# Kernel optimization log

Measured on AMD Instinct MI355X. Metric: run time of the kernel, lower is better.

Reference implementation:

```python
import jax, jax.numpy as jnp
import numpy as np

N_NODES = 100000
IN_F = 128
H_F = 128
LOOKBACK = 3
N_EDGES = 640000


def setup_inputs() -> dict:
    key = jax.random.key(0)
    ks = jax.random.split(key, 16)
    s = lambda k, shp: jax.random.normal(k, shp, dtype=jnp.float32) * 0.05
    inp = {
        "feat": jax.random.normal(ks[0], (N_NODES, IN_F), dtype=jnp.float32),
        "edges": jax.random.randint(ks[1], (LOOKBACK, 2, N_EDGES), 0, N_NODES, dtype=jnp.int32),
        # conv1 (SAGEConv pool, in->h) params
        "Wp1": s(ks[2], (IN_F, IN_F)), "bp1": jnp.zeros((IN_F,), jnp.float32),
        "Ws1": s(ks[3], (H_F, IN_F)), "Wn1": s(ks[4], (H_F, IN_F)), "b1": jnp.zeros((H_F,), jnp.float32),
        # BatchNorm1d affine params (training-mode batch stats)
        "gamma": jnp.ones((H_F,), jnp.float32), "beta": jnp.zeros((H_F,), jnp.float32),
        # conv2 (SAGEConv pool, h->h) params
        "Wp2": s(ks[5], (H_F, H_F)), "bp2": jnp.zeros((H_F,), jnp.float32),
        "Ws2": s(ks[6], (H_F, H_F)), "Wn2": s(ks[7], (H_F, H_F)), "b2": jnp.zeros((H_F,), jnp.float32),
    }
    return inp


def _sage_pool_conv(h, src, dst, Wp, bp, Ws, Wn, b):
    # pool aggregator: m = relu(fc_pool(h)); neigh = max over in-edges
    m = jax.nn.relu(h @ Wp.T + bp)                      # [N, d]
    agg = jax.ops.segment_max(m[src], dst, num_segments=N_NODES)  # [N, d]
    agg = jnp.where(jnp.isfinite(agg), agg, 0.0)        # nodes with no in-edges -> 0
    return h @ Ws.T + agg @ Wn.T + b


def _batchnorm(x, gamma, beta, eps=1e-5):
    mu = jnp.mean(x, axis=0)
    var = jnp.var(x, axis=0)
    return (x - mu) * jax.lax.rsqrt(var + eps) * gamma + beta


def reference(feat, edges, Wp1, bp1, Ws1, Wn1, b1, gamma, beta, Wp2, bp2, Ws2, Wn2, b2):
    def per_graph(e):
        src, dst = e[0], e[1]
        h = _sage_pool_conv(feat, src, dst, Wp1, bp1, Ws1, Wn1, b1)
        h = _batchnorm(h, gamma, beta)
        h = jax.nn.relu(h)
        h = _sage_pool_conv(h, src, dst, Wp2, bp2, Ws2, Wn2, b2)
        return h

    return jax.vmap(per_graph)(edges)  # [lookback, N, H_F]
```

## Files before the change

kernel.cpp:

```cpp
#include <hip/hip_runtime.h>
#include <hip/hip_bf16.h>

#define NNODES 100000
#define FD 128
#define NEDGES 640000
#define NB 391
#define NT64 1563
#define GX_TWOA 170
#define GX_ONEW 340
#define GX_HEAD 512
#define OFFS_U32 100032

typedef __bf16 bf16x8 __attribute__((ext_vector_type(8)));
typedef __bf16 bf16x4 __attribute__((ext_vector_type(4)));
typedef float f32x4 __attribute__((ext_vector_type(4)));
typedef unsigned short u16x8 __attribute__((ext_vector_type(8)));

__device__ __forceinline__ bf16x8 cvt8(float4 a, float4 b) {
  bf16x8 r;
  r[0] = (__bf16)a.x; r[1] = (__bf16)a.y; r[2] = (__bf16)a.z; r[3] = (__bf16)a.w;
  r[4] = (__bf16)b.x; r[5] = (__bf16)b.y; r[6] = (__bf16)b.z; r[7] = (__bf16)b.w;
  return r;
}

__device__ __forceinline__ void gl16(const void* g, void* l) {
  __builtin_amdgcn_global_load_lds(
      (const __attribute__((address_space(1))) unsigned int*)g,
      (__attribute__((address_space(3))) unsigned int*)l, 16, 0, 0);
}

__device__ __forceinline__ void stage_abf(const __bf16* A, long row0, int M,
                                          char* l, int wid, int lane) {
#pragma unroll
  for (int i = 0; i < 2; ++i) {
    const int r0 = wid * 8 + i * 4;
    const int rl = r0 + (lane >> 4);
    long row = row0 + rl;
    if (row > M - 1) row = M - 1;
    const int slot = (lane & 15) ^ (rl & 7);
    gl16((const char*)(A + row * FD) + slot * 16, l + r0 * 256);
  }
}

__device__ __forceinline__ void stage_a32(const float* A, long row0, int M,
                                          char* l, int wid, int lane) {
#pragma unroll
  for (int i = 0; i < 4; ++i) {
    const int r0 = wid * 8 + i * 2;
    const int rl = r0 + (lane >> 5);
    long row = row0 + rl;
    if (row > M - 1) row = M - 1;
    const int slot = (lane & 31) ^ (rl & 7);
    gl16((const char*)(A + row * FD) + slot * 16, l + r0 * 512);
  }
}

__global__ __launch_bounds__(256) void packw6_k(
    const float* __restrict__ W0, const float* __restrict__ W1,
    const float* __restrict__ W2, const float* __restrict__ W3,
    const float* __restrict__ W4, const float* __restrict__ W5,
    __bf16* __restrict__ out) {
  const int gidx = blockIdx.x * 256 + threadIdx.x;
  const int wi = gidx >> 11;
  const int f = gidx & 2047;
  const float* W = wi == 0 ? W0 : wi == 1 ? W1 : wi == 2 ? W2
                 : wi == 3 ? W3 : wi == 4 ? W4 : W5;
  const int c = f >> 8, kk = (f >> 6) & 3, lane = f & 63;
  const int lr = lane & 15, lg = lane >> 4;
  const float* p = W + (c * 16 + lr) * FD + kk * 32 + lg * 8;
  *(bf16x8*)(out + (long)gidx * 8) = cvt8(*(const float4*)p, *(const float4*)(p + 4));
}

template <int AM>
__device__ __forceinline__ void lds_arow(const char* l, int rl, int lg,
                                         const float* __restrict__ scsh,
                                         bf16x8 (&af)[4]) {
#pragma unroll
  for (int kk = 0; kk < 4; ++kk) {
    if constexpr (AM == 0) {
      const int s0 = kk * 8 + lg * 2;
      const float4 x = *(const float4*)(l + rl * 512 + ((s0 + 0) ^ (rl & 7)) * 16);
      const float4 y = *(const float4*)(l + rl * 512 + ((s0 + 1) ^ (rl & 7)) * 16);
      af[kk] = cvt8(x, y);
    } else {
      const int s = kk * 4 + lg;
      const bf16x8 r = *(const bf16x8*)(l + rl * 256 + (s ^ (rl & 7)) * 16);
      if constexpr (AM == 3) {
        const int k = lg * 8 + kk * 32;
        const float4 scx = *(const float4*)(scsh + k);
        const float4 scy = *(const float4*)(scsh + k + 4);
        const float4 shx = *(const float4*)(scsh + 128 + k);
        const float4 shy = *(const float4*)(scsh + 128 + k + 4);
        bf16x8 o;
        o[0] = (__bf16)fmaxf((float)r[0] * scx.x + shx.x, 0.f);
        o[1] = (__bf16)fmaxf((float)r[1] * scx.y + shx.y, 0.f);
        o[2] = (__bf16)fmaxf((float)r[2] * scx.z + shx.z, 0.f);
        o[3] = (__bf16)fmaxf((float)r[3] * scx.w + shx.w, 0.f);
        o[4] = (__bf16)fmaxf((float)r[4] * scy.x + shy.x, 0.f);
        o[5] = (__bf16)fmaxf((float)r[5] * scy.y + shy.y, 0.f);
        o[6] = (__bf16)fmaxf((float)r[6] * scy.z + shy.z, 0.f);
        o[7] = (__bf16)fmaxf((float)r[7] * scy.w + shy.w, 0.f);
        af[kk] = o;
      } else {
        af[kk] = r;
      }
    }
  }
}

template <int A0M, int A1M, bool TWOA, bool RELU, bool OUTBF16, bool STATS,
          bool WRITEB, bool NTOUT>
__global__ __launch_bounds__(512, 2) void gemm_k(
    const void* __restrict__ A0, long a0s, const void* __restrict__ A1, long a1s,
    const __bf16* __restrict__ W0p, const __bf16* __restrict__ W1p,
    const float* __restrict__ bias, const float* __restrict__ scsh0,
    void* __restrict__ outp, long os, float* __restrict__ pblk,
    __bf16* __restrict__ bcopy, int M) {
  constexpr int ASZ = (A0M == 0) ? 32768 : 16384;
  constexpr int A1SZ = TWOA ? 16384 : 0;
  constexpr int BSZ = ASZ + A1SZ;
  constexpr int LSZ = 2 * BSZ + (STATS ? 2048 : 0);
  __shared__ __align__(16) char lds[LSZ];
  float* s_red = (float*)(lds + 2 * BSZ);

  const int g = blockIdx.y;
  const int tid = threadIdx.x;
  const int wid = tid >> 6;
  const int lane = tid & 63;
  const int rw = wid & 1;
  const int cw = wid >> 1;
  const int lr = lane & 15;
  const int lg = lane >> 4;
  const int S = gridDim.x;

  const void* A0g = (const char*)A0 + (long)g * a0s;
  const void* A1g = (const char*)A1 + (TWOA ? (long)g * a1s : 0);
  void* outg = (char*)outp + (long)g * os;
  const float* scshg = (A0M == 3 || A1M == 3) ? scsh0 + (long)g * 256 : nullptr;

  bf16x8 bw0[2][4], bw1[2][4];
#pragma unroll
  for (int ci = 0; ci < 2; ++ci)
#pragma unroll
    for (int kk = 0; kk < 4; ++kk) {
      const long f = ((long)((cw * 2 + ci) * 4 + kk) * 64 + lane) * 8;
      bw0[ci][kk] = *(const bf16x8*)(W0p + f);
      if constexpr (TWOA) bw1[ci][kk] = *(const bf16x8*)(W1p + f);
    }

  float ps[2][4], pss[2][4];
  if constexpr (STATS) {
#pragma unroll
    for (int ci = 0; ci < 2; ++ci)
#pragma unroll
      for (int j = 0; j < 4; ++j) { ps[ci][j] = 0.f; pss[ci][j] = 0.f; }
  }

  auto stageA = [&](long t, char* buf) {
    if constexpr (A0M == 0) stage_a32((const float*)A0g, t * 64, M, buf, wid, lane);
    else stage_abf((const __bf16*)A0g, t * 64, M, buf, wid, lane);
    if constexpr (TWOA) stage_abf((const __bf16*)A1g, t * 64, M, buf + ASZ, wid, lane);
  };

  auto body = [&](long t, long tn, char* cur, char* nxt) {
    if (tn < NT64) stageA(tn, nxt);

    bf16x8 a0f[2][4];
#pragma unroll
    for (int tt = 0; tt < 2; ++tt)
      lds_arow<A0M>(cur, rw * 32 + tt * 16 + lr, lg, scshg, a0f[tt]);
    bf16x8 a1f[2][4];
    if constexpr (TWOA) {
#pragma unroll
      for (int tt = 0; tt < 2; ++tt)
        lds_arow<A1M>(cur + ASZ, rw * 32 + tt * 16 + lr, lg, scshg, a1f[tt]);
    }

    if constexpr (WRITEB) {
      if (cw == 0) {
#pragma unroll
        for (int tt = 0; tt < 2; ++tt) {
          const long row = t * 64 + rw * 32 + tt * 16 + lr;
          if (row < M)
#pragma unroll
            for (int kk = 0; kk < 4; ++kk)
              *(bf16x8*)(bcopy + row * FD + lg * 8 + kk * 32) = a0f[tt][kk];
        }
      }
    }

    f32x4 acc[2][2];
#pragma unroll
    for (int tt = 0; tt < 2; ++tt)
#pragma unroll
      for (int ci = 0; ci < 2; ++ci) acc[tt][ci] = (f32x4){0.f, 0.f, 0.f, 0.f};

#pragma unroll
    for (int ci = 0; ci < 2; ++ci)
#pragma unroll
      for (int tt = 0; tt < 2; ++tt)
#pragma unroll
        for (int kk = 0; kk < 4; ++kk)
          acc[tt][ci] = __builtin_amdgcn_mfma_f32_16x16x32_bf16(bw0[ci][kk], a0f[tt][kk], acc[tt][ci], 0, 0, 0);
    if constexpr (TWOA) {
#pragma unroll
      for (int ci = 0; ci < 2; ++ci)
#pragma unroll
        for (int tt = 0; tt < 2; ++tt)
#pragma unroll
          for (int kk = 0; kk < 4; ++kk)
            acc[tt][ci] = __builtin_amdgcn_mfma_f32_16x16x32_bf16(bw1[ci][kk], a1f[tt][kk], acc[tt][ci], 0, 0, 0);
    }

#pragma unroll
    for (int tt = 0; tt < 2; ++tt) {
      const long row = t * 64 + rw * 32 + tt * 16 + lr;
      const bool ok = row < M;
      f32x4 vv[2];
#pragma unroll
      for (int ci = 0; ci < 2; ++ci) {
        const int cb = cw * 32 + ci * 16 + lg * 4;
        f32x4 v = acc[tt][ci];
        if (bias) {
          const float4 bv = *(const float4*)(bias + cb);
          v[0] += bv.x; v[1] += bv.y; v[2] += bv.z; v[3] += bv.w;
        }
        if constexpr (STATS) {
          if (ok) {
#pragma unroll
            for (int j = 0; j < 4; ++j) { ps[ci][j] += v[j]; pss[ci][j] += v[j] * v[j]; }
          }
        }
        if constexpr (RELU) {
#pragma unroll
          for (int j = 0; j < 4; ++j) v[j] = fmaxf(v[j], 0.f);
        }
        vv[ci] = v;
      }
      if constexpr (OUTBF16) {
        bf16x4 o0, o1;
#pragma unroll
        for (int j = 0; j < 4; ++j) { o0[j] = (__bf16)vv[0][j]; o1[j] = (__bf16)vv[1][j]; }
        const int2 i0 = __builtin_bit_cast(int2, o0);
        const int2 i1 = __builtin_bit_cast(int2, o1);
        int2 p0, p1;
        p0.x = __shfl_xor(i0.x, 16); p0.y = __shfl_xor(i0.y, 16);
        p1.x = __shfl_xor(i1.x, 16); p1.y = __shfl_xor(i1.y, 16);
        int4 chunk;
        int cbase;
        if ((lg & 1) == 0) {
          chunk = (int4){i0.x, i0.y, p0.x, p0.y};
          cbase = cw * 32 + lg * 4;
        } else {
          chunk = (int4){p1.x, p1.y, i1.x, i1.y};
          cbase = cw * 32 + 16 + (lg - 1) * 4;
        }
        if (ok) *(int4*)((__bf16*)outg + row * FD + cbase) = chunk;
      } else {
        if (ok) {
#pragma unroll
          for (int ci = 0; ci < 2; ++ci) {
            const int cb = cw * 32 + ci * 16 + lg * 4;
            f32x4* p = (f32x4*)((float*)outg + row * FD + cb);
            if constexpr (NTOUT) __builtin_nontemporal_store(vv[ci], p);
            else *p = vv[ci];
          }
        }
      }
    }
    __syncthreads();
  };

  long t = blockIdx.x;
  stageA(t, lds);
  __syncthreads();

  for (;;) {
    long tn = t + S;
    body(t, tn, lds, lds + BSZ);
    t = tn;
    if (t >= NT64) break;
    tn = t + S;
    body(t, tn, lds + BSZ, lds);
    t = tn;
    if (t >= NT64) break;
  }

  if constexpr (STATS) {
#pragma unroll
    for (int ci = 0; ci < 2; ++ci)
#pragma unroll
      for (int j = 0; j < 4; ++j) {
        float s = ps[ci][j], q = pss[ci][j];
        s += __shfl_xor(s, 1); s += __shfl_xor(s, 2);
        s += __shfl_xor(s, 4); s += __shfl_xor(s, 8);
        q += __shfl_xor(q, 1); q += __shfl_xor(q, 2);
        q += __shfl_xor(q, 4); q += __shfl_xor(q, 8);
        if (lr == 0) {
          s_red[(0 * 8 + wid) * 32 + ci * 16 + lg * 4 + j] = s;
          s_red[(1 * 8 + wid) * 32 + ci * 16 + lg * 4 + j] = q;
        }
      }
    __syncthreads();
    if (tid < 256) {
      const int which = tid >> 7, col = tid & 127;
      const int cwi = col >> 5, cl = col & 31;
      const float a = s_red[(which * 8 + cwi * 2 + 0) * 32 + cl] +
                      s_red[(which * 8 + cwi * 2 + 1) * 32 + cl];
      pblk[((long)g * gridDim.x + blockIdx.x) * 256 + tid] = a;
    }
  }
}

__global__ __launch_bounds__(256) void bn_final2_k(const float* __restrict__ pblk,
                                                   const float* __restrict__ gamma,
                                                   const float* __restrict__ beta,
                                                   float* __restrict__ scsh3) {
  __shared__ float s_ss[128];
  const int g = blockIdx.y;
  const int tid = threadIdx.x;
  const float* p = pblk + (long)g * GX_TWOA * 256;
  float s = 0.f;
  for (int r = 0; r < GX_TWOA; ++r) s += p[r * 256 + tid];
  if (tid >= 128) s_ss[tid - 128] = s;
  __syncthreads();
  if (tid < 128) {
    const float mu = s / (float)NNODES;
    const float var = s_ss[tid] / (float)NNODES - mu * mu;
    const float sc = rsqrtf(var + 1e-5f) * gamma[tid];
    scsh3[g * 256 + tid] = sc;
    scsh3[g * 256 + 128 + tid] = beta[tid] - mu * sc;
  }
}


__global__ __launch_bounds__(256) void hist_rank3_k(const int* __restrict__ edges,
                                                    unsigned* __restrict__ deg3,
                                                    unsigned short* __restrict__ rank3) {
  const int g = blockIdx.y;
  const int e = blockIdx.x * 256 + threadIdx.x;
  if (e < NEDGES) {
    const int d = edges[(long)g * 2 * NEDGES + NEDGES + e];
    const unsigned r = atomicAdd(&deg3[(long)g * NNODES + d], 1u);
    rank3[(long)g * NEDGES + e] = (unsigned short)r;
  }
}

__global__ __launch_bounds__(256) void blocksum3_k(const unsigned* __restrict__ deg3,
                                                   unsigned* __restrict__ bsum3) {
  __shared__ unsigned s[256];
  const int g = blockIdx.y;
  const int i = blockIdx.x * 256 + threadIdx.x;
  s[threadIdx.x] = (i < NNODES) ? deg3[(long)g * NNODES + i] : 0u;
  __syncthreads();
#pragma unroll
  for (int o = 128; o > 0; o >>= 1) {
    if (threadIdx.x < o) s[threadIdx.x] += s[threadIdx.x + o];
    __syncthreads();
  }
  if (threadIdx.x == 0) bsum3[g * NB + blockIdx.x] = s[0];
}

__global__ __launch_bounds__(512) void scanb3_k(const unsigned* __restrict__ bsum3,
                                                unsigned* __restrict__ boffs3,
                                                unsigned* __restrict__ offs3) {
  __shared__ unsigned s[512];
  const int g = blockIdx.y;
  const unsigned v = (threadIdx.x < NB) ? bsum3[g * NB + threadIdx.x] : 0u;
  s[threadIdx.x] = v;
  __syncthreads();
#pragma unroll
  for (int o = 1; o < 512; o <<= 1) {
    unsigned t = (threadIdx.x >= o) ? s[threadIdx.x - o] : 0u;
    __syncthreads();
    s[threadIdx.x] += t;
    __syncthreads();
  }
  if (threadIdx.x < NB) boffs3[g * NB + threadIdx.x] = s[threadIdx.x] - v;
  if (threadIdx.x == 0) offs3[(long)g * OFFS_U32 + NNODES] = NEDGES;
}

__global__ __launch_bounds__(256) void offsets3_k(const unsigned* __restrict__ deg3,
                                                  const unsigned* __restrict__ boffs3,
                                                  unsigned* __restrict__ offs3) {
  __shared__ unsigned s[256];
  const int g = blockIdx.y;
  const int i = blockIdx.x * 256 + threadIdx.x;
  const unsigned v = (i < NNODES) ? deg3[(long)g * NNODES + i] : 0u;
  s[threadIdx.x] = v;
  __syncthreads();
#pragma unroll
  for (int o = 1; o < 256; o <<= 1) {
    unsigned t = (threadIdx.x >= o) ? s[threadIdx.x - o] : 0u;
    __syncthreads();
    s[threadIdx.x] += t;
    __syncthreads();
  }
  const unsigned excl = s[threadIdx.x] - v + boffs3[g * NB + blockIdx.x];
  if (i < NNODES) offs3[(long)g * OFFS_U32 + i] = excl;
}

__global__ __launch_bounds__(256) void scat3_k(const int* __restrict__ edges,
                                               const unsigned* __restrict__ offs3,
                                               const unsigned short* __restrict__ rank3,
                                               int* __restrict__ ssrc3) {
  const int g = blockIdx.y;
  const int e = blockIdx.x * 256 + threadIdx.x;
  if (e < NEDGES) {
    const int s = edges[(long)g * 2 * NEDGES + e];
    const int d = edges[(long)g * 2 * NEDGES + NEDGES + e];
    const unsigned p = offs3[(long)g * OFFS_U32 + d] + rank3[(long)g * NEDGES + e];
    ssrc3[(long)g * NEDGES + p] = s;
  }
}

__global__ __launch_bounds__(256) void agg_k(const unsigned short* __restrict__ m,
                                             long ms, const int* __restrict__ ssrc3,
                                             const unsigned* __restrict__ offs3,
                                             unsigned short* __restrict__ agg3) {
  const int g = blockIdx.y;
  const unsigned short* mg = m + (long)g * ms;
  const int* ssrc = ssrc3 + (long)g * NEDGES;
  const unsigned* offs = offs3 + (long)g * OFFS_U32;
  unsigned short* agg = agg3 + (long)g * NNODES * FD;

  const int gid = blockIdx.x * 256 + threadIdx.x;
  const int node = gid >> 4;
  if (node >= NNODES) return;
  const int fl = (gid & 15) * 8;
  const unsigned beg = offs[node], end = offs[node + 1];
  u16x8 acc = {0, 0, 0, 0, 0, 0, 0, 0};
  unsigned i = beg;
  for (; i + 2 <= end; i += 2) {
    const int s0 = ssrc[i];
    const int s1 = ssrc[i + 1];
    const u16x8 v0 = *(const u16x8*)(mg + (long)s0 * FD + fl);
    const u16x8 v1 = *(const u16x8*)(mg + (long)s1 * FD + fl);
#pragma unroll
    for (int j = 0; j < 8; ++j) {
      const unsigned short mx = v0[j] > v1[j] ? v0[j] : v1[j];
      acc[j] = mx > acc[j] ? mx : acc[j];
    }
  }
  if (i < end) {
    const u16x8 v = *(const u16x8*)(mg + (long)ssrc[i] * FD + fl);
#pragma unroll
    for (int j = 0; j < 8; ++j) acc[j] = v[j] > acc[j] ? v[j] : acc[j];
  }
  *(u16x8*)(agg + (long)node * FD + fl) = acc;
}

__global__ __launch_bounds__(256) void zero_k(float4* __restrict__ p, long n4) {
  const long i = (long)blockIdx.x * 256 + threadIdx.x;
  if (i < n4) p[i] = (float4){0.f, 0.f, 0.f, 0.f};
}

extern "C" void kernel_launch(void* const* d_in, const int* in_sizes, int n_in,
                              void* d_out, int out_size, void* d_ws, size_t ws_size,
                              hipStream_t stream) {
  const float* feat = (const float*)d_in[0];
  const int* edges = (const int*)d_in[1];
  const float* Wp1 = (const float*)d_in[2];
  const float* bp1 = (const float*)d_in[3];
  const float* Ws1 = (const float*)d_in[4];
  const float* Wn1 = (const float*)d_in[5];
  const float* b1 = (const float*)d_in[6];
  const float* gamma = (const float*)d_in[7];
  const float* beta = (const float*)d_in[8];
  const float* Wp2 = (const float*)d_in[9];
  const float* bp2 = (const float*)d_in[10];
  const float* Ws2 = (const float*)d_in[11];
  const float* Wn2 = (const float*)d_in[12];
  const float* b2 = (const float*)d_in[13];

  const long SZ_BF = 25600000;
  const long SZ_F32 = 51200000;

  char* w = (char*)d_ws;
  __bf16* m1 = (__bf16*)w;
  __bf16* featb = (__bf16*)(w + 25600000);
  __bf16* h1b3 = (__bf16*)(w + 51200000);
  __bf16* aggb3 = (__bf16*)(w + 128000000);
  __bf16* m2_3 = (__bf16*)(w + 204800000);
  float* pblk3 = (float*)(w + 204800000);
  __bf16* wpk = (__bf16*)(w + 281600000);
  float* scsh3 = (float*)(w + 281796608);
  unsigned* deg3 = (unsigned*)(w + 281799680);
  unsigned* offs3 = (unsigned*)(w + 282999680);
  unsigned* bsum3 = (unsigned*)(w + 284200064);
  unsigned* boffs3 = (unsigned*)(w + 284204928);
  unsigned short* rank3 = (unsigned short*)(w + 284209792);
  int* ssrc3 = (int*)(w + 288049792);

  __bf16* Wp1p = wpk;
  __bf16* Ws1p = wpk + 16384;
  __bf16* Wn1p = wpk + 2 * 16384;
  __bf16* Wp2p = wpk + 3 * 16384;
  __bf16* Ws2p = wpk + 4 * 16384;
  __bf16* Wn2p = wpk + 5 * 16384;

  const dim3 blk(256);
  const dim3 blk512(512);
  const int edgeGrid = (NEDGES + 255) / 256;
  const int aggGrid = (NNODES * 16 + 255) / 256;
  const int degZeroGrid = (3 * NNODES / 4 + 255) / 256;

  packw6_k<<<48, blk, 0, stream>>>(Wp1, Ws1, Wn1, Wp2, Ws2, Wn2, wpk);

  zero_k<<<degZeroGrid, blk, 0, stream>>>((float4*)deg3, 3L * NNODES / 4);
  hist_rank3_k<<<dim3(edgeGrid, 3), blk, 0, stream>>>(edges, deg3, rank3);
  blocksum3_k<<<dim3(NB, 3), blk, 0, stream>>>(deg3, bsum3);
  scanb3_k<<<dim3(1, 3), dim3(512), 0, stream>>>(bsum3, boffs3, offs3);
  offsets3_k<<<dim3(NB, 3), blk, 0, stream>>>(deg3, boffs3, offs3);
  scat3_k<<<dim3(edgeGrid, 3), blk, 0, stream>>>(edges, offs3, rank3, ssrc3);

  gemm_k<0, 0, false, true, true, false, true, false><<<dim3(GX_HEAD, 1), blk512, 0, stream>>>(
      feat, 0, nullptr, 0, Wp1p, nullptr, bp1, nullptr, m1, 0, nullptr, featb, NNODES);

  agg_k<<<dim3(aggGrid, 3), blk, 0, stream>>>((const unsigned short*)m1, 0L,
                                              ssrc3, offs3, (unsigned short*)aggb3);
  gemm_k<1, 1, true, false, true, true, false, false><<<dim3(GX_TWOA, 3), blk512, 0, stream>>>(
      aggb3, SZ_BF, featb, 0, Wn1p, Ws1p, b1, nullptr, h1b3, SZ_BF, pblk3, nullptr, NNODES);
  bn_final2_k<<<dim3(1, 3), blk, 0, stream>>>(pblk3, gamma, beta, scsh3);

  gemm_k<3, 0, false, true, true, false, false, false><<<dim3(GX_ONEW, 3), blk512, 0, stream>>>(
      h1b3, SZ_BF, nullptr, 0, Wp2p, nullptr, bp2, scsh3, m2_3, SZ_BF, nullptr, nullptr, NNODES);
  agg_k<<<dim3(aggGrid, 3), blk, 0, stream>>>((const unsigned short*)m2_3,
                                              (long)NNODES * FD, ssrc3, offs3,
                                              (unsigned short*)aggb3);
  gemm_k<3, 1, true, false, false, false, false, true><<<dim3(GX_TWOA, 3), blk512, 0, stream>>>(
      h1b3, SZ_BF, aggb3, SZ_BF, Ws2p, Wn2p, b2, scsh3, d_out, SZ_F32, nullptr, nullptr, NNODES);
}
```

Before: 485.4 us.

## Split each node's neighbor max across four edge groups per wavefront

```diff
diff --git a/kernel.cpp b/kernel.cpp
--- a/kernel.cpp
+++ b/kernel.cpp
@@ -424,18 +424,17 @@
   const unsigned* offs = offs3 + (long)g * OFFS_U32;
   unsigned short* agg = agg3 + (long)g * NNODES * FD;
 
-  const int gid = blockIdx.x * 256 + threadIdx.x;
-  const int node = gid >> 4;
-  if (node >= NNODES) return;
-  const int fl = (gid & 15) * 8;
+  const int node = blockIdx.x * 4 + (threadIdx.x >> 6);
+  const int lane = threadIdx.x & 63;
+  const int eg = lane >> 4;
+  const int fl = (lane & 15) * 8;
   const unsigned beg = offs[node], end = offs[node + 1];
+
   u16x8 acc = {0, 0, 0, 0, 0, 0, 0, 0};
-  unsigned i = beg;
-  for (; i + 2 <= end; i += 2) {
-    const int s0 = ssrc[i];
-    const int s1 = ssrc[i + 1];
-    const u16x8 v0 = *(const u16x8*)(mg + (long)s0 * FD + fl);
-    const u16x8 v1 = *(const u16x8*)(mg + (long)s1 * FD + fl);
+  unsigned i = beg + eg;
+  for (; i + 4 < end; i += 8) {
+    const u16x8 v0 = *(const u16x8*)(mg + (long)ssrc[i] * FD + fl);
+    const u16x8 v1 = *(const u16x8*)(mg + (long)ssrc[i + 4] * FD + fl);
 #pragma unroll
     for (int j = 0; j < 8; ++j) {
       const unsigned short mx = v0[j] > v1[j] ? v0[j] : v1[j];
@@ -447,7 +446,23 @@
 #pragma unroll
     for (int j = 0; j < 8; ++j) acc[j] = v[j] > acc[j] ? v[j] : acc[j];
   }
-  *(u16x8*)(agg + (long)node * FD + fl) = acc;
+
+  int4 a = __builtin_bit_cast(int4, acc);
+#pragma unroll
+  for (int mask = 16; mask <= 32; mask <<= 1) {
+    int4 o;
+    o.x = __shfl_xor(a.x, mask);
+    o.y = __shfl_xor(a.y, mask);
+    o.z = __shfl_xor(a.z, mask);
+    o.w = __shfl_xor(a.w, mask);
+    u16x8 A = __builtin_bit_cast(u16x8, a);
+    const u16x8 O = __builtin_bit_cast(u16x8, o);
+#pragma unroll
+    for (int j = 0; j < 8; ++j) A[j] = O[j] > A[j] ? O[j] : A[j];
+    a = __builtin_bit_cast(int4, A);
+  }
+  if (eg == 0)
+    *(u16x8*)(agg + (long)node * FD + fl) = __builtin_bit_cast(u16x8, a);
 }
 
 __global__ __launch_bounds__(256) void zero_k(float4* __restrict__ p, long n4) {
@@ -502,7 +517,6 @@
   const dim3 blk(256);
   const dim3 blk512(512);
   const int edgeGrid = (NEDGES + 255) / 256;
-  const int aggGrid = (NNODES * 16 + 255) / 256;
   const int degZeroGrid = (3 * NNODES / 4 + 255) / 256;
 
   packw6_k<<<48, blk, 0, stream>>>(Wp1, Ws1, Wn1, Wp2, Ws2, Wn2, wpk);
@@ -517,17 +531,17 @@
   gemm_k<0, 0, false, true, true, false, true, false><<<dim3(GX_HEAD, 1), blk512, 0, stream>>>(
       feat, 0, nullptr, 0, Wp1p, nullptr, bp1, nullptr, m1, 0, nullptr, featb, NNODES);
 
-  agg_k<<<dim3(aggGrid, 3), blk, 0, stream>>>((const unsigned short*)m1, 0L,
-                                              ssrc3, offs3, (unsigned short*)aggb3);
+  agg_k<<<dim3(25000, 3), blk, 0, stream>>>((const unsigned short*)m1, 0L,
+                                            ssrc3, offs3, (unsigned short*)aggb3);
   gemm_k<1, 1, true, false, true, true, false, false><<<dim3(GX_TWOA, 3), blk512, 0, stream>>>(
       aggb3, SZ_BF, featb, 0, Wn1p, Ws1p, b1, nullptr, h1b3, SZ_BF, pblk3, nullptr, NNODES);
   bn_final2_k<<<dim3(1, 3), blk, 0, stream>>>(pblk3, gamma, beta, scsh3);
 
   gemm_k<3, 0, false, true, true, false, false, false><<<dim3(GX_ONEW, 3), blk512, 0, stream>>>(
       h1b3, SZ_BF, nullptr, 0, Wp2p, nullptr, bp2, scsh3, m2_3, SZ_BF, nullptr, nullptr, NNODES);
-  agg_k<<<dim3(aggGrid, 3), blk, 0, stream>>>((const unsigned short*)m2_3,
-                                              (long)NNODES * FD, ssrc3, offs3,
-                                              (unsigned short*)aggb3);
+  agg_k<<<dim3(25000, 3), blk, 0, stream>>>((const unsigned short*)m2_3,
+                                            (long)NNODES * FD, ssrc3, offs3,
+                                            (unsigned short*)aggb3);
   gemm_k<3, 1, true, false, false, false, false, true><<<dim3(GX_TWOA, 3), blk512, 0, stream>>>(
       h1b3, SZ_BF, aggb3, SZ_BF, Ws2p, Wn2p, b2, scsh3, d_out, SZ_F32, nullptr, nullptr, NNODES);
 }
```

Result: slower. 523.5 us (+7.9%).

## Fuse edge histogram/rank into first GEMM launch as extra blocks

Applied to the files above, without the earlier changes.

```diff
diff --git a/kernel.cpp b/kernel.cpp
--- a/kernel.cpp
+++ b/kernel.cpp
@@ -9,6 +9,7 @@
 #define GX_TWOA 170
 #define GX_ONEW 340
 #define GX_HEAD 512
+#define HISTB 3750
 #define OFFS_U32 100032
 
 typedef __bf16 bf16x8 __attribute__((ext_vector_type(8)));
@@ -115,7 +116,9 @@
     const __bf16* __restrict__ W0p, const __bf16* __restrict__ W1p,
     const float* __restrict__ bias, const float* __restrict__ scsh0,
     void* __restrict__ outp, long os, float* __restrict__ pblk,
-    __bf16* __restrict__ bcopy, int M) {
+    __bf16* __restrict__ bcopy,
+    const int* __restrict__ hedges, unsigned* __restrict__ hdeg,
+    unsigned short* __restrict__ hrank, int histB, int M) {
   constexpr int ASZ = (A0M == 0) ? 32768 : 16384;
   constexpr int A1SZ = TWOA ? 16384 : 0;
   constexpr int BSZ = ASZ + A1SZ;
@@ -125,13 +128,33 @@
 
   const int g = blockIdx.y;
   const int tid = threadIdx.x;
+
+  int bx = blockIdx.x;
+  int S = gridDim.x;
+  if (histB > 0) {
+    const bool isGemm = (bx < 4096) && ((bx & 7) == 0);
+    if (!isGemm) {
+      const int hIdx = (bx < 4096) ? (bx - (bx >> 3) - 1) : (bx - GX_HEAD);
+      const long idx = (long)hIdx * 512 + tid;
+      if (idx < 3L * NEDGES) {
+        const int hg = (int)(idx / NEDGES);
+        const int e = (int)(idx - (long)hg * NEDGES);
+        const int d = hedges[(long)hg * 2 * NEDGES + NEDGES + e];
+        const unsigned r = atomicAdd(&hdeg[(long)hg * NNODES + d], 1u);
+        hrank[(long)hg * NEDGES + e] = (unsigned short)r;
+      }
+      return;
+    }
+    bx >>= 3;
+    S = GX_HEAD;
+  }
+
   const int wid = tid >> 6;
   const int lane = tid & 63;
   const int rw = wid & 1;
   const int cw = wid >> 1;
   const int lr = lane & 15;
   const int lg = lane >> 4;
-  const int S = gridDim.x;
 
   const void* A0g = (const char*)A0 + (long)g * a0s;
   const void* A1g = (const char*)A1 + (TWOA ? (long)g * a1s : 0);
@@ -271,7 +294,7 @@
     __syncthreads();
   };
 
-  long t = blockIdx.x;
+  long t = bx;
   stageA(t, lds);
   __syncthreads();
 
@@ -307,7 +330,7 @@
       const int cwi = col >> 5, cl = col & 31;
       const float a = s_red[(which * 8 + cwi * 2 + 0) * 32 + cl] +
                       s_red[(which * 8 + cwi * 2 + 1) * 32 + cl];
-      pblk[((long)g * gridDim.x + blockIdx.x) * 256 + tid] = a;
+      pblk[((long)g * S + bx) * 256 + tid] = a;
     }
   }
 }
@@ -333,18 +356,6 @@
   }
 }
 
-
-__global__ __launch_bounds__(256) void hist_rank3_k(const int* __restrict__ edges,
-                                                    unsigned* __restrict__ deg3,
-                                                    unsigned short* __restrict__ rank3) {
-  const int g = blockIdx.y;
-  const int e = blockIdx.x * 256 + threadIdx.x;
-  if (e < NEDGES) {
-    const int d = edges[(long)g * 2 * NEDGES + NEDGES + e];
-    const unsigned r = atomicAdd(&deg3[(long)g * NNODES + d], 1u);
-    rank3[(long)g * NEDGES + e] = (unsigned short)r;
-  }
-}
 
 __global__ __launch_bounds__(256) void blocksum3_k(const unsigned* __restrict__ deg3,
                                                    unsigned* __restrict__ bsum3) {
@@ -508,26 +519,31 @@
   packw6_k<<<48, blk, 0, stream>>>(Wp1, Ws1, Wn1, Wp2, Ws2, Wn2, wpk);
 
   zero_k<<<degZeroGrid, blk, 0, stream>>>((float4*)deg3, 3L * NNODES / 4);
-  hist_rank3_k<<<dim3(edgeGrid, 3), blk, 0, stream>>>(edges, deg3, rank3);
+
+  gemm_k<0, 0, false, true, true, false, true, false>
+      <<<dim3(GX_HEAD + HISTB, 1), blk512, 0, stream>>>(
+      feat, 0, nullptr, 0, Wp1p, nullptr, bp1, nullptr, m1, 0, nullptr, featb,
+      edges, deg3, rank3, HISTB, NNODES);
+
   blocksum3_k<<<dim3(NB, 3), blk, 0, stream>>>(deg3, bsum3);
   scanb3_k<<<dim3(1, 3), dim3(512), 0, stream>>>(bsum3, boffs3, offs3);
   offsets3_k<<<dim3(NB, 3), blk, 0, stream>>>(deg3, boffs3, offs3);
   scat3_k<<<dim3(edgeGrid, 3), blk, 0, stream>>>(edges, offs3, rank3, ssrc3);
 
-  gemm_k<0, 0, false, true, true, false, true, false><<<dim3(GX_HEAD, 1), blk512, 0, stream>>>(
-      feat, 0, nullptr, 0, Wp1p, nullptr, bp1, nullptr, m1, 0, nullptr, featb, NNODES);
-
   agg_k<<<dim3(aggGrid, 3), blk, 0, stream>>>((const unsigned short*)m1, 0L,
                                               ssrc3, offs3, (unsigned short*)aggb3);
   gemm_k<1, 1, true, false, true, true, false, false><<<dim3(GX_TWOA, 3), blk512, 0, stream>>>(
-      aggb3, SZ_BF, featb, 0, Wn1p, Ws1p, b1, nullptr, h1b3, SZ_BF, pblk3, nullptr, NNODES);
+      aggb3, SZ_BF, featb, 0, Wn1p, Ws1p, b1, nullptr, h1b3, SZ_BF, pblk3, nullptr,
+      nullptr, nullptr, nullptr, 0, NNODES);
   bn_final2_k<<<dim3(1, 3), blk, 0, stream>>>(pblk3, gamma, beta, scsh3);
 
   gemm_k<3, 0, false, true, true, false, false, false><<<dim3(GX_ONEW, 3), blk512, 0, stream>>>(
-      h1b3, SZ_BF, nullptr, 0, Wp2p, nullptr, bp2, scsh3, m2_3, SZ_BF, nullptr, nullptr, NNODES);
+      h1b3, SZ_BF, nullptr, 0, Wp2p, nullptr, bp2, scsh3, m2_3, SZ_BF, nullptr, nullptr,
+      nullptr, nullptr, nullptr, 0, NNODES);
   agg_k<<<dim3(aggGrid, 3), blk, 0, stream>>>((const unsigned short*)m2_3,
                                               (long)NNODES * FD, ssrc3, offs3,
                                               (unsigned short*)aggb3);
   gemm_k<3, 1, true, false, false, false, false, true><<<dim3(GX_TWOA, 3), blk512, 0, stream>>>(
-      h1b3, SZ_BF, aggb3, SZ_BF, Ws2p, Wn2p, b2, scsh3, d_out, SZ_F32, nullptr, nullptr, NNODES);
-}
+      h1b3, SZ_BF, aggb3, SZ_BF, Ws2p, Wn2p, b2, scsh3, d_out, SZ_F32, nullptr, nullptr,
+      nullptr, nullptr, nullptr, 0, NNODES);
+}
```

New measurement: 556.8 us. +14.7%, slower.
